# Kernel tuning notes

Measured on AMD Instinct MI355X. Metric: run time of the kernel, lower is better.

The kernel has to match this reference:

```python
import jax, jax.numpy as jnp
import numpy as np

N_HEADS = 8
HEAD_DIM = 48  # d_model 384 / 8 heads
D_MODEL = 384


def setup_inputs() -> dict:
    key = jax.random.key(0)
    k1, k2, k3, k4, k5 = jax.random.split(key, 5)
    B, S = 8, 2048
    return {
        "x": jax.random.normal(k1, (B, S, D_MODEL), dtype=jnp.float32),
        "W_qkv": jax.random.normal(k2, (3 * D_MODEL, D_MODEL), dtype=jnp.float32) * 0.02,
        "b_qkv": jax.random.normal(k3, (3 * D_MODEL,), dtype=jnp.float32) * 0.02,
        "W_o": jax.random.normal(k4, (D_MODEL, D_MODEL), dtype=jnp.float32) * 0.02,
        "b_o": jax.random.normal(k5, (D_MODEL,), dtype=jnp.float32) * 0.02,
    }


def reference(x, W_qkv, b_qkv, W_o, b_o):
    B, S, D = x.shape
    H, hd = N_HEADS, HEAD_DIM
    # fused QKV projection: [B,S,3D]
    qkv = jnp.einsum("bsd,ed->bse", x, W_qkv) + b_qkv
    # [B,S,H,3*hd] -> [B,H,S,3*hd]
    qkv = qkv.reshape(B, S, H, 3 * hd).transpose(0, 2, 1, 3)
    Q, K, V = jnp.split(qkv, 3, axis=-1)  # each [B,H,S,hd]
    scale = 1.0 / np.sqrt(hd).astype(np.float32)
    scores = jnp.einsum("bhqd,bhkd->bhqk", Q, K) * scale  # [B,H,S,S]
    # NOTE: original softmaxes over dim=1 (heads), not the key dim
    attn = jax.nn.softmax(scores, axis=1)
    values = jnp.einsum("bhqk,bhkd->bhqd", attn, V)  # [B,H,S,hd]
    # NOTE: original reshapes [B,H,S,hd] directly to [B,S,H*hd] (no permute back)
    values = values.reshape(B, S, H * hd)
    out = jnp.einsum("bsd,ed->bse", values, W_o) + b_o
    return out
```

## Files before the change

### kernel.cpp

```cpp
#include <hip/hip_runtime.h>
#include <hip/hip_bf16.h>

#define BB 8
#define SS 2048
#define DD 384
#define HH 8
#define HD 48
#define QT 32
#define KT 32

typedef unsigned short u16;
typedef unsigned short u16x4 __attribute__((ext_vector_type(4)));
typedef unsigned short u16x8 __attribute__((ext_vector_type(8)));
typedef short s16x8 __attribute__((ext_vector_type(8)));
typedef float f32x4 __attribute__((ext_vector_type(4)));

__device__ __forceinline__ float bf2f(u16 v){
  union { unsigned int u; float f; } x; x.u = ((unsigned int)v) << 16; return x.f;
}
__device__ __forceinline__ u16 f2bf(float f){
  union { float f; unsigned int u; } x; x.f = f;
  unsigned int r = x.u + 0x7fffu + ((x.u >> 16) & 1u);
  return (u16)(r >> 16);
}
__device__ __forceinline__ u16 f2bf_trunc(float f){
  union { float f; unsigned int u; } x; x.f = f;
  return (u16)(x.u >> 16);
}
__device__ __forceinline__ void split2(float f, u16& h, u16& l){
  union { float f; unsigned int u; } x; x.f = f;
  h = (u16)(x.u >> 16);
  l = f2bf(f - bf2f(h));
}

#define LBAR() do { \
  asm volatile("s_waitcnt lgkmcnt(0)" ::: "memory"); \
  __builtin_amdgcn_s_barrier(); \
  asm volatile("" ::: "memory"); \
} while (0)

__global__ __launch_bounds__(512, 4) void qkv_gemm(
    const float* __restrict__ x, const float* __restrict__ W,
    const float* __restrict__ bias,
    u16* __restrict__ Q, u16* __restrict__ Kd, u16* __restrict__ Vt)
{
  __shared__ u16 Ah[128][40], Al[128][40], Bh[128][40], Bl[128][40];
  const int tid  = threadIdx.x;
  const int w    = tid >> 6, lane = tid & 63;
  const int lg   = lane >> 4, ln = lane & 15;
  const int wm   = w >> 1, wn = w & 1;
  const int mb   = blockIdx.x / 9, nb = blockIdx.x % 9;
  const int m0   = mb * 128, n0 = nb * 128;
  const int srow = tid >> 3, sk4 = (tid & 7) << 2;
  const float qscale = 0.14433756729740643f;

  f32x4 acc[8];
  #pragma unroll
  for (int i = 0; i < 8; i++) acc[i] = (f32x4){0.f,0.f,0.f,0.f};

  for (int ks = 0; ks < 12; ks++){
    const int k0 = ks * 32;
    __syncthreads();
    #pragma unroll
    for (int p = 0; p < 2; p++){
      const int row = srow + p*64;
      float4 av = *(const float4*)(x + (long)(m0+row)*DD + k0 + sk4);
      float4 bv = *(const float4*)(W + (long)(n0+row)*DD + k0 + sk4);
      u16 h0,l0,h1,l1,h2,l2,h3,l3;
      split2(av.x,h0,l0); split2(av.y,h1,l1); split2(av.z,h2,l2); split2(av.w,h3,l3);
      *(u16x4*)&Ah[row][sk4] = (u16x4){h0,h1,h2,h3};
      *(u16x4*)&Al[row][sk4] = (u16x4){l0,l1,l2,l3};
      split2(bv.x,h0,l0); split2(bv.y,h1,l1); split2(bv.z,h2,l2); split2(bv.w,h3,l3);
      *(u16x4*)&Bh[row][sk4] = (u16x4){h0,h1,h2,h3};
      *(u16x4*)&Bl[row][sk4] = (u16x4){l0,l1,l2,l3};
    }
    __syncthreads();
    s16x8 bh[4], bl[4];
    #pragma unroll
    for (int fn = 0; fn < 4; fn++){
      const int br = wn*64 + fn*16 + ln;
      bh[fn] = *(const s16x8*)&Bh[br][lg*8];
      bl[fn] = *(const s16x8*)&Bl[br][lg*8];
    }
    #pragma unroll
    for (int fm = 0; fm < 2; fm++){
      const int ar = wm*32 + fm*16 + ln;
      s16x8 ah = *(const s16x8*)&Ah[ar][lg*8];
      s16x8 al = *(const s16x8*)&Al[ar][lg*8];
      #pragma unroll
      for (int fn = 0; fn < 4; fn++){
        f32x4 c = acc[fm*4+fn];
        c = __builtin_amdgcn_mfma_f32_16x16x32_bf16(ah, bh[fn], c, 0, 0, 0);
        c = __builtin_amdgcn_mfma_f32_16x16x32_bf16(ah, bl[fn], c, 0, 0, 0);
        c = __builtin_amdgcn_mfma_f32_16x16x32_bf16(al, bh[fn], c, 0, 0, 0);
        acc[fm*4+fn] = c;
      }
    }
  }
  #pragma unroll
  for (int fm = 0; fm < 2; fm++){
    #pragma unroll
    for (int fn = 0; fn < 4; fn++){
      const int e = n0 + wn*64 + fn*16 + ln;
      const float bi = bias[e];
      const int h = e / 144, c = e % 144;
      #pragma unroll
      for (int r = 0; r < 4; r++){
        const int mm = m0 + wm*32 + fm*16 + lg*4 + r;
        const int bb = mm >> 11, s = mm & 2047;
        const float v = acc[fm*4+fn][r] + bi;
        if (c < 48){
          Q[(((long)(bb*HH + h))*SS + s)*HD + c] = f2bf(v * qscale);
        } else if (c < 96){
          Kd[(((long)(bb*HH + h))*SS + s)*HD + (c-48)] = f2bf(v);
        } else {
          Vt[(((long)(bb*HH + h))*HD + (c-96))*SS + s] = f2bf(v);
        }
      }
    }
  }
}

__global__ __launch_bounds__(512, 4) void attn_kernel(
    const u16* __restrict__ Q, const u16* __restrict__ K,
    const u16* __restrict__ Vg, float* __restrict__ vals)
{
  __shared__ float Ss[HH][QT][36];
  __shared__ u16  Pb[HH][QT][40];

  const int tid  = threadIdx.x;
  const int h    = tid >> 6;
  const int lane = tid & 63;
  const int wg   = ((int)blockIdx.x % 8) * 64 + (int)blockIdx.x / 8;
  const int b    = wg >> 6;
  const int qt   = wg & 63;
  const int q0   = qt * QT;
  const int lg   = lane >> 4;
  const int ln   = lane & 15;

  const long hbase = ((long)(b*HH + h)) * SS;
  const u16* vbase = Vg + ((long)(b*HH + h)) * HD * SS;

  s16x8 qf0[2], qf1[2];
  #pragma unroll
  for (int qs = 0; qs < 2; qs++){
    const u16* qp = Q + (hbase + q0 + qs*16 + ln)*HD;
    qf0[qs] = *(const s16x8*)(qp + lg*8);
    if (lane < 32) qf1[qs] = *(const s16x8*)(qp + 32 + lg*8);
    else           qf1[qs] = (s16x8){0,0,0,0,0,0,0,0};
  }

  f32x4 oacc[2][3];
  #pragma unroll
  for (int qs = 0; qs < 2; qs++)
    #pragma unroll
    for (int c = 0; c < 3; c++) oacc[qs][c] = (f32x4){0.f,0.f,0.f,0.f};

  const int sq0 = tid >> 5, sk = tid & 31;

  for (int kt = 0; kt < SS/KT; kt++){
    const int k0 = kt * KT;

    s16x8 vf[3];
    #pragma unroll
    for (int c = 0; c < 3; c++)
      vf[c] = *(const s16x8*)(vbase + (long)(c*16 + ln)*SS + k0 + lg*8);

    #pragma unroll
    for (int nt = 0; nt < 2; nt++){
      const u16* kp = K + (hbase + k0 + nt*16 + ln)*HD;
      s16x8 kf0 = *(const s16x8*)(kp + lg*8);
      s16x8 kf1;
      if (lane < 32) kf1 = *(const s16x8*)(kp + 32 + lg*8);
      else           kf1 = (s16x8){0,0,0,0,0,0,0,0};
      #pragma unroll
      for (int qs = 0; qs < 2; qs++){
        f32x4 a = (f32x4){0.f,0.f,0.f,0.f};
        a = __builtin_amdgcn_mfma_f32_16x16x32_bf16(kf0, qf0[qs], a, 0, 0, 0);
        a = __builtin_amdgcn_mfma_f32_16x16x32_bf16(kf1, qf1[qs], a, 0, 0, 0);
        *(f32x4*)&Ss[h][qs*16 + ln][nt*16 + lg*4] = a;
      }
    }
    LBAR();

    #pragma unroll
    for (int i = 0; i < 2; i++){
      const int sq = sq0 + i*16;
      float e0 = __expf(Ss[0][sq][sk]), e1 = __expf(Ss[1][sq][sk]);
      float e2 = __expf(Ss[2][sq][sk]), e3 = __expf(Ss[3][sq][sk]);
      float e4 = __expf(Ss[4][sq][sk]), e5 = __expf(Ss[5][sq][sk]);
      float e6 = __expf(Ss[6][sq][sk]), e7 = __expf(Ss[7][sq][sk]);
      float rs = 1.f / (e0+e1+e2+e3+e4+e5+e6+e7);
      Pb[0][sq][sk] = f2bf_trunc(e0*rs); Pb[1][sq][sk] = f2bf_trunc(e1*rs);
      Pb[2][sq][sk] = f2bf_trunc(e2*rs); Pb[3][sq][sk] = f2bf_trunc(e3*rs);
      Pb[4][sq][sk] = f2bf_trunc(e4*rs); Pb[5][sq][sk] = f2bf_trunc(e5*rs);
      Pb[6][sq][sk] = f2bf_trunc(e6*rs); Pb[7][sq][sk] = f2bf_trunc(e7*rs);
    }
    LBAR();

    #pragma unroll
    for (int qs = 0; qs < 2; qs++){
      s16x8 pf = *(const s16x8*)&Pb[h][qs*16 + ln][lg*8];
      #pragma unroll
      for (int c = 0; c < 3; c++)
        oacc[qs][c] = __builtin_amdgcn_mfma_f32_16x16x32_bf16(pf, vf[c], oacc[qs][c], 0, 0, 0);
    }
  }

  float* op = vals + (hbase + q0)*HD;
  #pragma unroll
  for (int qs = 0; qs < 2; qs++)
    #pragma unroll
    for (int c = 0; c < 3; c++)
      #pragma unroll
      for (int r = 0; r < 4; r++)
        op[(long)(qs*16 + lg*4 + r)*HD + c*16 + ln] = oacc[qs][c][r];
}

__global__ __launch_bounds__(512, 4) void out_gemm(
    const float* __restrict__ A, const float* __restrict__ W,
    const float* __restrict__ bias, float* __restrict__ out)
{
  __shared__ u16 Ah[128][40], Al[128][40], Bh[128][40], Bl[128][40];
  const int tid  = threadIdx.x;
  const int w    = tid >> 6, lane = tid & 63;
  const int lg   = lane >> 4, ln = lane & 15;
  const int wm   = w >> 1, wn = w & 1;
  const int mb   = blockIdx.x / 3, nb = blockIdx.x % 3;
  const int m0   = mb * 128, n0 = nb * 128;
  const int srow = tid >> 3, sk4 = (tid & 7) << 2;

  f32x4 acc[8];
  #pragma unroll
  for (int i = 0; i < 8; i++) acc[i] = (f32x4){0.f,0.f,0.f,0.f};

  for (int ks = 0; ks < 12; ks++){
    const int k0 = ks * 32;
    __syncthreads();
    #pragma unroll
    for (int p = 0; p < 2; p++){
      const int row = srow + p*64;
      float4 av = *(const float4*)(A + (long)(m0+row)*DD + k0 + sk4);
      float4 bv = *(const float4*)(W + (long)(n0+row)*DD + k0 + sk4);
      u16 h0,l0,h1,l1,h2,l2,h3,l3;
      split2(av.x,h0,l0); split2(av.y,h1,l1); split2(av.z,h2,l2); split2(av.w,h3,l3);
      *(u16x4*)&Ah[row][sk4] = (u16x4){h0,h1,h2,h3};
      *(u16x4*)&Al[row][sk4] = (u16x4){l0,l1,l2,l3};
      split2(bv.x,h0,l0); split2(bv.y,h1,l1); split2(bv.z,h2,l2); split2(bv.w,h3,l3);
      *(u16x4*)&Bh[row][sk4] = (u16x4){h0,h1,h2,h3};
      *(u16x4*)&Bl[row][sk4] = (u16x4){l0,l1,l2,l3};
    }
    __syncthreads();
    s16x8 bh[4], bl[4];
    #pragma unroll
    for (int fn = 0; fn < 4; fn++){
      const int br = wn*64 + fn*16 + ln;
      bh[fn] = *(const s16x8*)&Bh[br][lg*8];
      bl[fn] = *(const s16x8*)&Bl[br][lg*8];
    }
    #pragma unroll
    for (int fm = 0; fm < 2; fm++){
      const int ar = wm*32 + fm*16 + ln;
      s16x8 ah = *(const s16x8*)&Ah[ar][lg*8];
      s16x8 al = *(const s16x8*)&Al[ar][lg*8];
      #pragma unroll
      for (int fn = 0; fn < 4; fn++){
        f32x4 c = acc[fm*4+fn];
        c = __builtin_amdgcn_mfma_f32_16x16x32_bf16(ah, bh[fn], c, 0, 0, 0);
        c = __builtin_amdgcn_mfma_f32_16x16x32_bf16(ah, bl[fn], c, 0, 0, 0);
        c = __builtin_amdgcn_mfma_f32_16x16x32_bf16(al, bh[fn], c, 0, 0, 0);
        acc[fm*4+fn] = c;
      }
    }
  }
  #pragma unroll
  for (int fm = 0; fm < 2; fm++){
    #pragma unroll
    for (int fn = 0; fn < 4; fn++){
      const int e = n0 + wn*64 + fn*16 + ln;
      const float bi = bias[e];
      #pragma unroll
      for (int r = 0; r < 4; r++){
        const int mm = m0 + wm*32 + fm*16 + lg*4 + r;
        out[(long)mm*DD + e] = acc[fm*4+fn][r] + bi;
      }
    }
  }
}

extern "C" void kernel_launch(void* const* d_in, const int* in_sizes, int n_in,
                              void* d_out, int out_size, void* d_ws, size_t ws_size,
                              hipStream_t stream)
{
  const float* x    = (const float*)d_in[0];
  const float* Wqkv = (const float*)d_in[1];
  const float* bqkv = (const float*)d_in[2];
  const float* Wo   = (const float*)d_in[3];
  const float* bo   = (const float*)d_in[4];
  float* out = (float*)d_out;

  const size_t QSZ = (size_t)BB*HH*SS*HD;
  u16* Q  = (u16*)d_ws;
  u16* K  = Q + QSZ;
  u16* Vt = K + QSZ;
  float* vals = (float*)(Vt + QSZ);

  qkv_gemm<<<1152, 512, 0, stream>>>(x, Wqkv, bqkv, Q, K, Vt);
  attn_kernel<<<512, 512, 0, stream>>>(Q, K, Vt, vals);
  out_gemm<<<384, 512, 0, stream>>>(vals, Wo, bo, out);
}
```

Before: 262.3 us.

## Double-buffer K fragments, use exp2 with prescaled Q, and raise MFMA priority

The attention loop now prefetches the next tile's K fragments into a second register buffer and unrolls by two, so global K loads overlap with the current tile's MFMAs and softmax. The Q scale is folded with log2(e), which lets the softmax use the hardware exp2 and rcp intrinsics instead of __expf and a full division. The MFMA sections are wrapped in s_setprio to favour matrix issue across waves. The cost is higher register pressure from the doubled K buffers, plus one wasted prefetch at the end (index wraps via the mask) and slightly lower precision from the fast rcp.

```diff
diff --git a/kernel.cpp b/kernel.cpp
--- a/kernel.cpp
+++ b/kernel.cpp
@@ -52,7 +52,7 @@
   const int mb   = blockIdx.x / 9, nb = blockIdx.x % 9;
   const int m0   = mb * 128, n0 = nb * 128;
   const int srow = tid >> 3, sk4 = (tid & 7) << 2;
-  const float qscale = 0.14433756729740643f;
+  const float qscale = 0.2082350972f;
 
   f32x4 acc[8];
   #pragma unroll
@@ -140,6 +140,7 @@
 
   const long hbase = ((long)(b*HH + h)) * SS;
   const u16* vbase = Vg + ((long)(b*HH + h)) * HD * SS;
+  const s16x8 z8 = (s16x8){0,0,0,0,0,0,0,0};
 
   s16x8 qf0[2], qf1[2];
   #pragma unroll
@@ -147,7 +148,7 @@
     const u16* qp = Q + (hbase + q0 + qs*16 + ln)*HD;
     qf0[qs] = *(const s16x8*)(qp + lg*8);
     if (lane < 32) qf1[qs] = *(const s16x8*)(qp + 32 + lg*8);
-    else           qf1[qs] = (s16x8){0,0,0,0,0,0,0,0};
+    else           qf1[qs] = z8;
   }
 
   f32x4 oacc[2][3];
@@ -158,54 +159,79 @@
 
   const int sq0 = tid >> 5, sk = tid & 31;
 
-  for (int kt = 0; kt < SS/KT; kt++){
-    const int k0 = kt * KT;
-
-    s16x8 vf[3];
-    #pragma unroll
-    for (int c = 0; c < 3; c++)
-      vf[c] = *(const s16x8*)(vbase + (long)(c*16 + ln)*SS + k0 + lg*8);
-
-    #pragma unroll
-    for (int nt = 0; nt < 2; nt++){
-      const u16* kp = K + (hbase + k0 + nt*16 + ln)*HD;
-      s16x8 kf0 = *(const s16x8*)(kp + lg*8);
-      s16x8 kf1;
-      if (lane < 32) kf1 = *(const s16x8*)(kp + 32 + lg*8);
-      else           kf1 = (s16x8){0,0,0,0,0,0,0,0};
-      #pragma unroll
-      for (int qs = 0; qs < 2; qs++){
-        f32x4 a = (f32x4){0.f,0.f,0.f,0.f};
-        a = __builtin_amdgcn_mfma_f32_16x16x32_bf16(kf0, qf0[qs], a, 0, 0, 0);
-        a = __builtin_amdgcn_mfma_f32_16x16x32_bf16(kf1, qf1[qs], a, 0, 0, 0);
-        *(f32x4*)&Ss[h][qs*16 + ln][nt*16 + lg*4] = a;
-      }
-    }
-    LBAR();
-
-    #pragma unroll
-    for (int i = 0; i < 2; i++){
-      const int sq = sq0 + i*16;
-      float e0 = __expf(Ss[0][sq][sk]), e1 = __expf(Ss[1][sq][sk]);
-      float e2 = __expf(Ss[2][sq][sk]), e3 = __expf(Ss[3][sq][sk]);
-      float e4 = __expf(Ss[4][sq][sk]), e5 = __expf(Ss[5][sq][sk]);
-      float e6 = __expf(Ss[6][sq][sk]), e7 = __expf(Ss[7][sq][sk]);
-      float rs = 1.f / (e0+e1+e2+e3+e4+e5+e6+e7);
-      Pb[0][sq][sk] = f2bf_trunc(e0*rs); Pb[1][sq][sk] = f2bf_trunc(e1*rs);
-      Pb[2][sq][sk] = f2bf_trunc(e2*rs); Pb[3][sq][sk] = f2bf_trunc(e3*rs);
-      Pb[4][sq][sk] = f2bf_trunc(e4*rs); Pb[5][sq][sk] = f2bf_trunc(e5*rs);
-      Pb[6][sq][sk] = f2bf_trunc(e6*rs); Pb[7][sq][sk] = f2bf_trunc(e7*rs);
-    }
-    LBAR();
-
-    #pragma unroll
-    for (int qs = 0; qs < 2; qs++){
-      s16x8 pf = *(const s16x8*)&Pb[h][qs*16 + ln][lg*8];
-      #pragma unroll
-      for (int c = 0; c < 3; c++)
-        oacc[qs][c] = __builtin_amdgcn_mfma_f32_16x16x32_bf16(pf, vf[c], oacc[qs][c], 0, 0, 0);
-    }
-  }
+  s16x8 kfA[2][2], kfB[2][2];
+  int k0 = 0;
+  #pragma unroll
+  for (int nt = 0; nt < 2; nt++){
+    const u16* kp = K + (hbase + nt*16 + ln)*HD;
+    kfA[0][nt] = *(const s16x8*)(kp + lg*8);
+    if (lane < 32) kfB[0][nt] = *(const s16x8*)(kp + 32 + lg*8);
+    else           kfB[0][nt] = z8;
+  }
+
+#define STEP(CUR, NXT) { \
+     \
+    s16x8 vf0 = *(const s16x8*)(vbase + (long)(     ln)*SS + k0 + lg*8); \
+    s16x8 vf1 = *(const s16x8*)(vbase + (long)(16 + ln)*SS + k0 + lg*8); \
+    s16x8 vf2 = *(const s16x8*)(vbase + (long)(32 + ln)*SS + k0 + lg*8); \
+     \
+    const int knx = (k0 + KT) & (SS - 1); \
+    _Pragma("unroll") \
+    for (int nt = 0; nt < 2; nt++){ \
+      const u16* kp = K + (hbase + knx + nt*16 + ln)*HD; \
+      kfA[NXT][nt] = *(const s16x8*)(kp + lg*8); \
+      if (lane < 32) kfB[NXT][nt] = *(const s16x8*)(kp + 32 + lg*8); \
+      else           kfB[NXT][nt] = z8; \
+    } \
+     \
+    __builtin_amdgcn_s_setprio(1); \
+    _Pragma("unroll") \
+    for (int nt = 0; nt < 2; nt++){ \
+      _Pragma("unroll") \
+      for (int qs = 0; qs < 2; qs++){ \
+        f32x4 a = (f32x4){0.f,0.f,0.f,0.f}; \
+        a = __builtin_amdgcn_mfma_f32_16x16x32_bf16(kfA[CUR][nt], qf0[qs], a, 0, 0, 0); \
+        a = __builtin_amdgcn_mfma_f32_16x16x32_bf16(kfB[CUR][nt], qf1[qs], a, 0, 0, 0); \
+        *(f32x4*)&Ss[h][qs*16 + ln][nt*16 + lg*4] = a; \
+      } \
+    } \
+    __builtin_amdgcn_s_setprio(0); \
+    LBAR();    \
+    _Pragma("unroll") \
+    for (int i = 0; i < 2; i++){ \
+      const int sq = sq0 + i*16; \
+      float e0 = __builtin_amdgcn_exp2f(Ss[0][sq][sk]); \
+      float e1 = __builtin_amdgcn_exp2f(Ss[1][sq][sk]); \
+      float e2 = __builtin_amdgcn_exp2f(Ss[2][sq][sk]); \
+      float e3 = __builtin_amdgcn_exp2f(Ss[3][sq][sk]); \
+      float e4 = __builtin_amdgcn_exp2f(Ss[4][sq][sk]); \
+      float e5 = __builtin_amdgcn_exp2f(Ss[5][sq][sk]); \
+      float e6 = __builtin_amdgcn_exp2f(Ss[6][sq][sk]); \
+      float e7 = __builtin_amdgcn_exp2f(Ss[7][sq][sk]); \
+      float rs = __builtin_amdgcn_rcpf(((e0+e1)+(e2+e3))+((e4+e5)+(e6+e7))); \
+      Pb[0][sq][sk] = f2bf_trunc(e0*rs); Pb[1][sq][sk] = f2bf_trunc(e1*rs); \
+      Pb[2][sq][sk] = f2bf_trunc(e2*rs); Pb[3][sq][sk] = f2bf_trunc(e3*rs); \
+      Pb[4][sq][sk] = f2bf_trunc(e4*rs); Pb[5][sq][sk] = f2bf_trunc(e5*rs); \
+      Pb[6][sq][sk] = f2bf_trunc(e6*rs); Pb[7][sq][sk] = f2bf_trunc(e7*rs); \
+    } \
+    LBAR();    \
+    __builtin_amdgcn_s_setprio(1); \
+    _Pragma("unroll") \
+    for (int qs = 0; qs < 2; qs++){ \
+      s16x8 pf = *(const s16x8*)&Pb[h][qs*16 + ln][lg*8]; \
+      oacc[qs][0] = __builtin_amdgcn_mfma_f32_16x16x32_bf16(pf, vf0, oacc[qs][0], 0, 0, 0); \
+      oacc[qs][1] = __builtin_amdgcn_mfma_f32_16x16x32_bf16(pf, vf1, oacc[qs][1], 0, 0, 0); \
+      oacc[qs][2] = __builtin_amdgcn_mfma_f32_16x16x32_bf16(pf, vf2, oacc[qs][2], 0, 0, 0); \
+    } \
+    __builtin_amdgcn_s_setprio(0); \
+    k0 = knx; \
+  }
+
+  for (int kt2 = 0; kt2 < SS/KT/2; kt2++){
+    STEP(0, 1)
+    STEP(1, 0)
+  }
+#undef STEP
 
   float* op = vals + (hbase + q0)*HD;
   #pragma unroll
```

New measurement: 222.8 us, median of 2. -15.1%, faster.

## Double-buffer attention scores, store bf16 logits, use exp2 with folded log2e scale

Applied to the files above, without the earlier changes.

The attention loop now double-buffers the score and probability tiles in shared memory. The QK^T MFMAs for the next key tile are issued before the cross-head softmax of the current tile, which removes one barrier per iteration. Scores are stored as truncated bf16 pairs instead of fp32, which halves LDS traffic. The Q scale now folds in log2(e), so the softmax can use the hardware exp2 and rcp instructions, and s_setprio hints are placed around the MFMA sections. The cost is lower precision in the logits and more LDS footprint for the two buffers.

```diff
diff --git a/kernel.cpp b/kernel.cpp
--- a/kernel.cpp
+++ b/kernel.cpp
@@ -10,27 +10,28 @@
 #define KT 32
 
 typedef unsigned short u16;
+typedef unsigned int u32;
 typedef unsigned short u16x4 __attribute__((ext_vector_type(4)));
 typedef unsigned short u16x8 __attribute__((ext_vector_type(8)));
 typedef short s16x8 __attribute__((ext_vector_type(8)));
 typedef float f32x4 __attribute__((ext_vector_type(4)));
 
 __device__ __forceinline__ float bf2f(u16 v){
-  union { unsigned int u; float f; } x; x.u = ((unsigned int)v) << 16; return x.f;
+  union { u32 u; float f; } x; x.u = ((u32)v) << 16; return x.f;
 }
 __device__ __forceinline__ u16 f2bf(float f){
-  union { float f; unsigned int u; } x; x.f = f;
-  unsigned int r = x.u + 0x7fffu + ((x.u >> 16) & 1u);
+  union { float f; u32 u; } x; x.f = f;
+  u32 r = x.u + 0x7fffu + ((x.u >> 16) & 1u);
   return (u16)(r >> 16);
 }
-__device__ __forceinline__ u16 f2bf_trunc(float f){
-  union { float f; unsigned int u; } x; x.f = f;
-  return (u16)(x.u >> 16);
-}
 __device__ __forceinline__ void split2(float f, u16& h, u16& l){
-  union { float f; unsigned int u; } x; x.f = f;
+  union { float f; u32 u; } x; x.f = f;
   h = (u16)(x.u >> 16);
   l = f2bf(f - bf2f(h));
+}
+__device__ __forceinline__ u32 pack_trunc2(float a, float b){
+  union { float f; u32 u; } xa, xb; xa.f = a; xb.f = b;
+  return (xa.u >> 16) | (xb.u & 0xffff0000u);
 }
 
 #define LBAR() do { \
@@ -52,7 +53,7 @@
   const int mb   = blockIdx.x / 9, nb = blockIdx.x % 9;
   const int m0   = mb * 128, n0 = nb * 128;
   const int srow = tid >> 3, sk4 = (tid & 7) << 2;
-  const float qscale = 0.14433756729740643f;
+  const float qscale = 0.2082350972f;
 
   f32x4 acc[8];
   #pragma unroll
@@ -125,8 +126,8 @@
     const u16* __restrict__ Q, const u16* __restrict__ K,
     const u16* __restrict__ Vg, float* __restrict__ vals)
 {
-  __shared__ float Ss[HH][QT][36];
-  __shared__ u16  Pb[HH][QT][40];
+  __shared__ u16 Ss[2][HH][QT][36];
+  __shared__ u16 Pb[2][HH][QT][40];
 
   const int tid  = threadIdx.x;
   const int h    = tid >> 6;
@@ -140,6 +141,7 @@
 
   const long hbase = ((long)(b*HH + h)) * SS;
   const u16* vbase = Vg + ((long)(b*HH + h)) * HD * SS;
+  const s16x8 z8 = (s16x8){0,0,0,0,0,0,0,0};
 
   s16x8 qf0[2], qf1[2];
   #pragma unroll
@@ -147,7 +149,7 @@
     const u16* qp = Q + (hbase + q0 + qs*16 + ln)*HD;
     qf0[qs] = *(const s16x8*)(qp + lg*8);
     if (lane < 32) qf1[qs] = *(const s16x8*)(qp + 32 + lg*8);
-    else           qf1[qs] = (s16x8){0,0,0,0,0,0,0,0};
+    else           qf1[qs] = z8;
   }
 
   f32x4 oacc[2][3];
@@ -156,56 +158,76 @@
     #pragma unroll
     for (int c = 0; c < 3; c++) oacc[qs][c] = (f32x4){0.f,0.f,0.f,0.f};
 
-  const int sq0 = tid >> 5, sk = tid & 31;
-
-  for (int kt = 0; kt < SS/KT; kt++){
-    const int k0 = kt * KT;
-
-    s16x8 vf[3];
-    #pragma unroll
-    for (int c = 0; c < 3; c++)
-      vf[c] = *(const s16x8*)(vbase + (long)(c*16 + ln)*SS + k0 + lg*8);
-
-    #pragma unroll
-    for (int nt = 0; nt < 2; nt++){
-      const u16* kp = K + (hbase + k0 + nt*16 + ln)*HD;
-      s16x8 kf0 = *(const s16x8*)(kp + lg*8);
-      s16x8 kf1;
-      if (lane < 32) kf1 = *(const s16x8*)(kp + 32 + lg*8);
-      else           kf1 = (s16x8){0,0,0,0,0,0,0,0};
-      #pragma unroll
-      for (int qs = 0; qs < 2; qs++){
-        f32x4 a = (f32x4){0.f,0.f,0.f,0.f};
-        a = __builtin_amdgcn_mfma_f32_16x16x32_bf16(kf0, qf0[qs], a, 0, 0, 0);
-        a = __builtin_amdgcn_mfma_f32_16x16x32_bf16(kf1, qf1[qs], a, 0, 0, 0);
-        *(f32x4*)&Ss[h][qs*16 + ln][nt*16 + lg*4] = a;
-      }
-    }
+  const int smq = tid >> 4, smk = (tid & 15) << 1;
+
+#define QKT(cbx, k0x) { \
+    __builtin_amdgcn_s_setprio(1); \
+    _Pragma("unroll") \
+    for (int nt = 0; nt < 2; nt++){ \
+      const u16* kp = K + (hbase + (k0x) + nt*16 + ln)*HD; \
+      s16x8 kf0 = *(const s16x8*)(kp + lg*8); \
+      s16x8 kf1; \
+      if (lane < 32) kf1 = *(const s16x8*)(kp + 32 + lg*8); \
+      else           kf1 = z8; \
+      _Pragma("unroll") \
+      for (int qs = 0; qs < 2; qs++){ \
+        f32x4 a = (f32x4){0.f,0.f,0.f,0.f}; \
+        a = __builtin_amdgcn_mfma_f32_16x16x32_bf16(kf0, qf0[qs], a, 0, 0, 0); \
+        a = __builtin_amdgcn_mfma_f32_16x16x32_bf16(kf1, qf1[qs], a, 0, 0, 0); \
+        u32 w0 = pack_trunc2(a[0], a[1]); \
+        u32 w1 = pack_trunc2(a[2], a[3]); \
+        u32* dst = (u32*)&Ss[cbx][h][qs*16 + ln][nt*16 + lg*4]; \
+        dst[0] = w0; dst[1] = w1; \
+      } \
+    } \
+    __builtin_amdgcn_s_setprio(0); \
+  }
+
+  QKT(0, 0)
+  LBAR();
+
+  int cb = 0, k0 = 0;
+  for (int t = 0; t < SS/KT; t++){
+    s16x8 vf0 = *(const s16x8*)(vbase + (long)(     ln)*SS + k0 + lg*8);
+    s16x8 vf1 = *(const s16x8*)(vbase + (long)(16 + ln)*SS + k0 + lg*8);
+    s16x8 vf2 = *(const s16x8*)(vbase + (long)(32 + ln)*SS + k0 + lg*8);
+
+    if (t < SS/KT - 1) QKT(cb^1, k0 + KT)
+
+    {
+      float e0[8], e1[8];
+      float sum0 = 0.f, sum1 = 0.f;
+      #pragma unroll
+      for (int hh = 0; hh < 8; hh++){
+        u32 wv = *(const u32*)&Ss[cb][hh][smq][smk];
+        union { u32 u; float f; } a0, a1;
+        a0.u = wv << 16; a1.u = wv & 0xffff0000u;
+        e0[hh] = __builtin_amdgcn_exp2f(a0.f);
+        e1[hh] = __builtin_amdgcn_exp2f(a1.f);
+        sum0 += e0[hh]; sum1 += e1[hh];
+      }
+      float r0 = __builtin_amdgcn_rcpf(sum0);
+      float r1 = __builtin_amdgcn_rcpf(sum1);
+      #pragma unroll
+      for (int hh = 0; hh < 8; hh++)
+        *(u32*)&Pb[cb][hh][smq][smk] = pack_trunc2(e0[hh]*r0, e1[hh]*r1);
+    }
+
     LBAR();
 
-    #pragma unroll
-    for (int i = 0; i < 2; i++){
-      const int sq = sq0 + i*16;
-      float e0 = __expf(Ss[0][sq][sk]), e1 = __expf(Ss[1][sq][sk]);
-      float e2 = __expf(Ss[2][sq][sk]), e3 = __expf(Ss[3][sq][sk]);
-      float e4 = __expf(Ss[4][sq][sk]), e5 = __expf(Ss[5][sq][sk]);
-      float e6 = __expf(Ss[6][sq][sk]), e7 = __expf(Ss[7][sq][sk]);
-      float rs = 1.f / (e0+e1+e2+e3+e4+e5+e6+e7);
-      Pb[0][sq][sk] = f2bf_trunc(e0*rs); Pb[1][sq][sk] = f2bf_trunc(e1*rs);
-      Pb[2][sq][sk] = f2bf_trunc(e2*rs); Pb[3][sq][sk] = f2bf_trunc(e3*rs);
-      Pb[4][sq][sk] = f2bf_trunc(e4*rs); Pb[5][sq][sk] = f2bf_trunc(e5*rs);
-      Pb[6][sq][sk] = f2bf_trunc(e6*rs); Pb[7][sq][sk] = f2bf_trunc(e7*rs);
-    }
-    LBAR();
-
+    __builtin_amdgcn_s_setprio(1);
     #pragma unroll
     for (int qs = 0; qs < 2; qs++){
-      s16x8 pf = *(const s16x8*)&Pb[h][qs*16 + ln][lg*8];
-      #pragma unroll
-      for (int c = 0; c < 3; c++)
-        oacc[qs][c] = __builtin_amdgcn_mfma_f32_16x16x32_bf16(pf, vf[c], oacc[qs][c], 0, 0, 0);
-    }
-  }
+      s16x8 pf = *(const s16x8*)&Pb[cb][h][qs*16 + ln][lg*8];
+      oacc[qs][0] = __builtin_amdgcn_mfma_f32_16x16x32_bf16(pf, vf0, oacc[qs][0], 0, 0, 0);
+      oacc[qs][1] = __builtin_amdgcn_mfma_f32_16x16x32_bf16(pf, vf1, oacc[qs][1], 0, 0, 0);
+      oacc[qs][2] = __builtin_amdgcn_mfma_f32_16x16x32_bf16(pf, vf2, oacc[qs][2], 0, 0, 0);
+    }
+    __builtin_amdgcn_s_setprio(0);
+
+    cb ^= 1; k0 += KT;
+  }
+#undef QKT
 
   float* op = vals + (hbase + q0)*HD;
   #pragma unroll
```

Result: faster. 249.9 us (-4.7%).

## Repartition attention warps by query/key slice so head softmax stays in registers

Applied to the files above, without the earlier changes.

Each warp now computes scores for all 8 heads of one 16x16 query/key sub-tile, so the cross-head softmax runs entirely in registers using exp2 (log2e is folded into the Q scale) and a fast reciprocal. This removes the fp32 score round-trip through shared memory and one of the two barriers per tile. The key tile is doubled to 64 and the probability buffer is double-buffered. The cost is more registers (8 heads of Q and K fragments), which drops the occupancy hint to 2, plus redundant K loads across warps.

```diff
diff --git a/kernel.cpp b/kernel.cpp
--- a/kernel.cpp
+++ b/kernel.cpp
@@ -7,30 +7,32 @@
 #define HH 8
 #define HD 48
 #define QT 32
-#define KT 32
+#define KT 64
 
 typedef unsigned short u16;
+typedef unsigned int u32;
 typedef unsigned short u16x4 __attribute__((ext_vector_type(4)));
 typedef unsigned short u16x8 __attribute__((ext_vector_type(8)));
+typedef unsigned int u32x2 __attribute__((ext_vector_type(2)));
 typedef short s16x8 __attribute__((ext_vector_type(8)));
 typedef float f32x4 __attribute__((ext_vector_type(4)));
 
 __device__ __forceinline__ float bf2f(u16 v){
-  union { unsigned int u; float f; } x; x.u = ((unsigned int)v) << 16; return x.f;
+  union { u32 u; float f; } x; x.u = ((u32)v) << 16; return x.f;
 }
 __device__ __forceinline__ u16 f2bf(float f){
-  union { float f; unsigned int u; } x; x.f = f;
-  unsigned int r = x.u + 0x7fffu + ((x.u >> 16) & 1u);
+  union { float f; u32 u; } x; x.f = f;
+  u32 r = x.u + 0x7fffu + ((x.u >> 16) & 1u);
   return (u16)(r >> 16);
 }
-__device__ __forceinline__ u16 f2bf_trunc(float f){
-  union { float f; unsigned int u; } x; x.f = f;
-  return (u16)(x.u >> 16);
-}
 __device__ __forceinline__ void split2(float f, u16& h, u16& l){
-  union { float f; unsigned int u; } x; x.f = f;
+  union { float f; u32 u; } x; x.f = f;
   h = (u16)(x.u >> 16);
   l = f2bf(f - bf2f(h));
+}
+__device__ __forceinline__ u32 pack_trunc2(float a, float b){
+  union { float f; u32 u; } xa, xb; xa.f = a; xb.f = b;
+  return (xa.u >> 16) | (xb.u & 0xffff0000u);
 }
 
 #define LBAR() do { \
@@ -52,7 +54,7 @@
   const int mb   = blockIdx.x / 9, nb = blockIdx.x % 9;
   const int m0   = mb * 128, n0 = nb * 128;
   const int srow = tid >> 3, sk4 = (tid & 7) << 2;
-  const float qscale = 0.14433756729740643f;
+  const float qscale = 0.2082350972f;
 
   f32x4 acc[8];
   #pragma unroll
@@ -109,112 +111,133 @@
         const int mm = m0 + wm*32 + fm*16 + lg*4 + r;
         const int bb = mm >> 11, s = mm & 2047;
         const float v = acc[fm*4+fn][r] + bi;
-        if (c < 48){
-          Q[(((long)(bb*HH + h))*SS + s)*HD + c] = f2bf(v * qscale);
-        } else if (c < 96){
-          Kd[(((long)(bb*HH + h))*SS + s)*HD + (c-48)] = f2bf(v);
-        } else {
-          Vt[(((long)(bb*HH + h))*HD + (c-96))*SS + s] = f2bf(v);
-        }
-      }
-    }
-  }
-}
-
-__global__ __launch_bounds__(512, 4) void attn_kernel(
+        if (c < 48)       Q[(((long)(bb*HH + h))*SS + s)*HD + c] = f2bf(v * qscale);
+        else if (c < 96)  Kd[(((long)(bb*HH + h))*SS + s)*HD + (c-48)] = f2bf(v);
+        else              Vt[(((long)(bb*HH + h))*HD + (c-96))*SS + s] = f2bf(v);
+      }
+    }
+  }
+}
+
+__global__ __launch_bounds__(512, 2) void attn_kernel(
     const u16* __restrict__ Q, const u16* __restrict__ K,
     const u16* __restrict__ Vg, float* __restrict__ vals)
 {
-  __shared__ float Ss[HH][QT][36];
-  __shared__ u16  Pb[HH][QT][40];
+  __shared__ u16 Pb[2][HH][QT][72];
 
   const int tid  = threadIdx.x;
-  const int h    = tid >> 6;
+  const int w    = tid >> 6;
   const int lane = tid & 63;
-  const int wg   = ((int)blockIdx.x % 8) * 64 + (int)blockIdx.x / 8;
-  const int b    = wg >> 6;
-  const int qt   = wg & 63;
-  const int q0   = qt * QT;
   const int lg   = lane >> 4;
   const int ln   = lane & 15;
-
-  const long hbase = ((long)(b*HH + h)) * SS;
-  const u16* vbase = Vg + ((long)(b*HH + h)) * HD * SS;
-
-  s16x8 qf0[2], qf1[2];
-  #pragma unroll
-  for (int qs = 0; qs < 2; qs++){
-    const u16* qp = Q + (hbase + q0 + qs*16 + ln)*HD;
-    qf0[qs] = *(const s16x8*)(qp + lg*8);
-    if (lane < 32) qf1[qs] = *(const s16x8*)(qp + 32 + lg*8);
-    else           qf1[qs] = (s16x8){0,0,0,0,0,0,0,0};
+  const int qs   = w >> 2;
+  const int ksl  = w & 3;
+  const int h    = w;
+
+  const int wg = ((int)blockIdx.x % 8) * 64 + (int)blockIdx.x / 8;
+  const int b  = wg >> 6;
+  const int qt = wg & 63;
+  const int q0 = qt * QT;
+
+  const long bh0   = (long)(b*HH);
+  const long hbase = (bh0 + h) * SS;
+  const u16* vbase = Vg + (bh0 + h) * HD * SS;
+  const s16x8 z8 = (s16x8){0,0,0,0,0,0,0,0};
+
+  s16x8 qfA[8], qfB[8];
+  #pragma unroll
+  for (int h2 = 0; h2 < 8; h2++){
+    const u16* qp = Q + ((bh0 + h2)*SS + q0 + qs*16 + ln)*HD;
+    qfA[h2] = *(const s16x8*)(qp + lg*8);
+    if (lane < 32) qfB[h2] = *(const s16x8*)(qp + 32 + lg*8);
+    else           qfB[h2] = z8;
   }
 
   f32x4 oacc[2][3];
   #pragma unroll
-  for (int qs = 0; qs < 2; qs++)
-    #pragma unroll
-    for (int c = 0; c < 3; c++) oacc[qs][c] = (f32x4){0.f,0.f,0.f,0.f};
-
-  const int sq0 = tid >> 5, sk = tid & 31;
-
-  for (int kt = 0; kt < SS/KT; kt++){
-    const int k0 = kt * KT;
-
-    s16x8 vf[3];
+  for (int q2 = 0; q2 < 2; q2++)
+    #pragma unroll
+    for (int c = 0; c < 3; c++) oacc[q2][c] = (f32x4){0.f,0.f,0.f,0.f};
+
+  int cb = 0;
+  for (int t = 0; t < SS/KT; t++){
+    const int k0 = t * KT;
+    const int kk = k0 + ksl*16;
+
+    s16x8 kA[8], kB[8];
+    #pragma unroll
+    for (int h2 = 0; h2 < 8; h2++){
+      const u16* kp = K + ((bh0 + h2)*SS + kk + ln)*HD;
+      kA[h2] = *(const s16x8*)(kp + lg*8);
+      if (lane < 32) kB[h2] = *(const s16x8*)(kp + 32 + lg*8);
+      else           kB[h2] = z8;
+    }
+
+    f32x4 sc[8];
+    __builtin_amdgcn_s_setprio(1);
+    #pragma unroll
+    for (int h2 = 0; h2 < 8; h2++){
+      f32x4 a = (f32x4){0.f,0.f,0.f,0.f};
+      a = __builtin_amdgcn_mfma_f32_16x16x32_bf16(kA[h2], qfA[h2], a, 0, 0, 0);
+      a = __builtin_amdgcn_mfma_f32_16x16x32_bf16(kB[h2], qfB[h2], a, 0, 0, 0);
+      sc[h2] = a;
+    }
+    __builtin_amdgcn_s_setprio(0);
+
+    s16x8 vf[3][2];
     #pragma unroll
     for (int c = 0; c < 3; c++)
-      vf[c] = *(const s16x8*)(vbase + (long)(c*16 + ln)*SS + k0 + lg*8);
-
-    #pragma unroll
-    for (int nt = 0; nt < 2; nt++){
-      const u16* kp = K + (hbase + k0 + nt*16 + ln)*HD;
-      s16x8 kf0 = *(const s16x8*)(kp + lg*8);
-      s16x8 kf1;
-      if (lane < 32) kf1 = *(const s16x8*)(kp + 32 + lg*8);
-      else           kf1 = (s16x8){0,0,0,0,0,0,0,0};
-      #pragma unroll
-      for (int qs = 0; qs < 2; qs++){
-        f32x4 a = (f32x4){0.f,0.f,0.f,0.f};
-        a = __builtin_amdgcn_mfma_f32_16x16x32_bf16(kf0, qf0[qs], a, 0, 0, 0);
-        a = __builtin_amdgcn_mfma_f32_16x16x32_bf16(kf1, qf1[qs], a, 0, 0, 0);
-        *(f32x4*)&Ss[h][qs*16 + ln][nt*16 + lg*4] = a;
-      }
+      #pragma unroll
+      for (int ks2 = 0; ks2 < 2; ks2++)
+        vf[c][ks2] = *(const s16x8*)(vbase + (long)(c*16 + ln)*SS + k0 + ks2*32 + lg*8);
+
+    #pragma unroll
+    for (int r = 0; r < 4; r++){
+      float e0 = __builtin_amdgcn_exp2f(sc[0][r]);
+      float e1 = __builtin_amdgcn_exp2f(sc[1][r]);
+      float e2 = __builtin_amdgcn_exp2f(sc[2][r]);
+      float e3 = __builtin_amdgcn_exp2f(sc[3][r]);
+      float e4 = __builtin_amdgcn_exp2f(sc[4][r]);
+      float e5 = __builtin_amdgcn_exp2f(sc[5][r]);
+      float e6 = __builtin_amdgcn_exp2f(sc[6][r]);
+      float e7 = __builtin_amdgcn_exp2f(sc[7][r]);
+      float rs = __builtin_amdgcn_rcpf(((e0+e1)+(e2+e3))+((e4+e5)+(e6+e7)));
+      sc[0][r] = e0*rs; sc[1][r] = e1*rs; sc[2][r] = e2*rs; sc[3][r] = e3*rs;
+      sc[4][r] = e4*rs; sc[5][r] = e5*rs; sc[6][r] = e6*rs; sc[7][r] = e7*rs;
+    }
+
+    #pragma unroll
+    for (int h2 = 0; h2 < 8; h2++){
+      u32x2 pw;
+      pw[0] = pack_trunc2(sc[h2][0], sc[h2][1]);
+      pw[1] = pack_trunc2(sc[h2][2], sc[h2][3]);
+      *(u32x2*)&Pb[cb][h2][qs*16 + ln][ksl*16 + lg*4] = pw;
     }
     LBAR();
 
-    #pragma unroll
-    for (int i = 0; i < 2; i++){
-      const int sq = sq0 + i*16;
-      float e0 = __expf(Ss[0][sq][sk]), e1 = __expf(Ss[1][sq][sk]);
-      float e2 = __expf(Ss[2][sq][sk]), e3 = __expf(Ss[3][sq][sk]);
-      float e4 = __expf(Ss[4][sq][sk]), e5 = __expf(Ss[5][sq][sk]);
-      float e6 = __expf(Ss[6][sq][sk]), e7 = __expf(Ss[7][sq][sk]);
-      float rs = 1.f / (e0+e1+e2+e3+e4+e5+e6+e7);
-      Pb[0][sq][sk] = f2bf_trunc(e0*rs); Pb[1][sq][sk] = f2bf_trunc(e1*rs);
-      Pb[2][sq][sk] = f2bf_trunc(e2*rs); Pb[3][sq][sk] = f2bf_trunc(e3*rs);
-      Pb[4][sq][sk] = f2bf_trunc(e4*rs); Pb[5][sq][sk] = f2bf_trunc(e5*rs);
-      Pb[6][sq][sk] = f2bf_trunc(e6*rs); Pb[7][sq][sk] = f2bf_trunc(e7*rs);
-    }
-    LBAR();
-
-    #pragma unroll
-    for (int qs = 0; qs < 2; qs++){
-      s16x8 pf = *(const s16x8*)&Pb[h][qs*16 + ln][lg*8];
-      #pragma unroll
-      for (int c = 0; c < 3; c++)
-        oacc[qs][c] = __builtin_amdgcn_mfma_f32_16x16x32_bf16(pf, vf[c], oacc[qs][c], 0, 0, 0);
-    }
+    __builtin_amdgcn_s_setprio(1);
+    #pragma unroll
+    for (int q2 = 0; q2 < 2; q2++){
+      #pragma unroll
+      for (int ks2 = 0; ks2 < 2; ks2++){
+        s16x8 pf = *(const s16x8*)&Pb[cb][h][q2*16 + ln][ks2*32 + lg*8];
+        oacc[q2][0] = __builtin_amdgcn_mfma_f32_16x16x32_bf16(pf, vf[0][ks2], oacc[q2][0], 0, 0, 0);
+        oacc[q2][1] = __builtin_amdgcn_mfma_f32_16x16x32_bf16(pf, vf[1][ks2], oacc[q2][1], 0, 0, 0);
+        oacc[q2][2] = __builtin_amdgcn_mfma_f32_16x16x32_bf16(pf, vf[2][ks2], oacc[q2][2], 0, 0, 0);
+      }
+    }
+    __builtin_amdgcn_s_setprio(0);
+    cb ^= 1;
   }
 
   float* op = vals + (hbase + q0)*HD;
   #pragma unroll
-  for (int qs = 0; qs < 2; qs++)
+  for (int q2 = 0; q2 < 2; q2++)
     #pragma unroll
     for (int c = 0; c < 3; c++)
       #pragma unroll
       for (int r = 0; r < 4; r++)
-        op[(long)(qs*16 + lg*4 + r)*HD + c*16 + ln] = oacc[qs][c][r];
+        op[(long)(q2*16 + lg*4 + r)*HD + c*16 + ln] = oacc[q2][c][r];
 }
 
 __global__ __launch_bounds__(512, 4) void out_gemm(
```

Result: slower. 271.3 us (+3.4%).
